# Kernel optimization log

Measured on AMD Instinct MI355X. Metric: run time of the kernel, lower is better.

## Reference

```python
import jax, jax.numpy as jnp
import numpy as np

HID = 256   # hidden_size
NH = 8      # n_heads
DH = HID // NH  # head dim = 32
NV = 20     # num_variables
B, T = 32, 512
EPS = 1e-5


def _ln(x, g, b):
    mu = jnp.mean(x, axis=-1, keepdims=True)
    var = jnp.mean(jnp.square(x - mu), axis=-1, keepdims=True)
    return (x - mu) * jax.lax.rsqrt(var + EPS) * g + b


def setup_inputs() -> dict:
    key = jax.random.key(0)
    ks = jax.random.split(key, 20)
    s = 0.05  # xavier-ish scale for random weights
    return {
        "x": jax.random.normal(ks[0], (B, T, NV, HID), dtype=jnp.float32),
        "cls_token": jax.random.normal(ks[1], (HID,), dtype=jnp.float32) * s,
        "wq": jax.random.normal(ks[2], (HID, HID), dtype=jnp.float32) * s,
        "bq": jnp.zeros((HID,), jnp.float32),
        "wk": jax.random.normal(ks[3], (HID, HID), dtype=jnp.float32) * s,
        "bk": jnp.zeros((HID,), jnp.float32),
        "wv": jax.random.normal(ks[4], (HID, HID), dtype=jnp.float32) * s,
        "bv": jnp.zeros((HID,), jnp.float32),
        "wo": jax.random.normal(ks[5], (HID, HID), dtype=jnp.float32) * s,
        "bo": jnp.zeros((HID,), jnp.float32),
        "ln1_g": jnp.ones((HID,), jnp.float32),
        "ln1_b": jnp.zeros((HID,), jnp.float32),
        "w1": jax.random.normal(ks[6], (HID, 4 * HID), dtype=jnp.float32) * s,
        "b1": jnp.zeros((4 * HID,), jnp.float32),
        "w2": jax.random.normal(ks[7], (4 * HID, HID), dtype=jnp.float32) * s,
        "b2": jnp.zeros((HID,), jnp.float32),
        "ln2_g": jnp.ones((HID,), jnp.float32),
        "ln2_b": jnp.zeros((HID,), jnp.float32),
        "ww": jax.random.normal(ks[8], (HID, NV), dtype=jnp.float32) * s,
        "bw": jnp.zeros((NV,), jnp.float32),
    }


def reference(x, cls_token, wq, bq, wk, bk, wv, bv, wo, bo,
              ln1_g, ln1_b, w1, b1, w2, b2, ln2_g, ln2_b, ww, bw):
    # x: [B, T, V, H] -- stacked pre-projected variables (input_size == hidden_size,
    # so the torch module has no per-variable projections).
    b, t = x.shape[0], x.shape[1]
    scale = 1.0 / np.sqrt(DH)

    # Cross-attention: query = cls token (len 1), keys/values = variables (len V).
    # No static_context, so the query is shared across (b, t).
    q = (cls_token @ wq + bq).reshape(NH, DH)            # [H] -> [nh, dh]
    k = (x @ wk + bk).reshape(b, t, NV, NH, DH)          # [B,T,V,nh,dh]
    v = (x @ wv + bv).reshape(b, t, NV, NH, DH)
    scores = jnp.einsum('hd,btvhd->bthv', q, k) * scale  # [B,T,nh,V]
    attn = jax.nn.softmax(scores, axis=-1)
    ctx = jnp.einsum('bthv,btvhd->bthd', attn, v).reshape(b, t, HID)
    attn_out = ctx @ wo + bo                             # [B,T,H]

    # FF block: LN -> Linear(4H) -> GELU -> Linear(H) -> LN (dropout is eval no-op)
    h = _ln(attn_out, ln1_g, ln1_b)
    h = jax.nn.gelu(h @ w1 + b1, approximate=False)
    h = h @ w2 + b2
    processed = _ln(h, ln2_g, ln2_b)                     # [B,T,H]

    weights = jax.nn.softmax(processed @ ww + bw, axis=-1)   # [B,T,V]
    vs_output = jnp.einsum('btv,btvh->bth', weights, x)      # [B,T,H]
    return vs_output, weights
```

## Files before the change

### kernel.cpp

```cpp
#include <hip/hip_runtime.h>
#include <hip/hip_bf16.h>
#include <math.h>

#define BT   16384
#define HIDS 256
#define NHS  8
#define NVS  20

typedef __attribute__((ext_vector_type(8))) short short8;
typedef __attribute__((ext_vector_type(4))) float floatx4;

__device__ __forceinline__ float bf2f(unsigned int u) {
    union { unsigned int u; float f; } cv; cv.u = u << 16; return cv.f;
}
__device__ __forceinline__ unsigned short f2bf(float f) {
    union { __hip_bfloat16 h; unsigned short u; } cv; cv.h = __float2bfloat16(f); return cv.u;
}
__device__ __forceinline__ unsigned int pk2(float a, float b) {
    return (unsigned int)f2bf(a) | ((unsigned int)f2bf(b) << 16);
}
__device__ __forceinline__ void gload16(const void* g, void* l) {
    __builtin_amdgcn_global_load_lds(
        (const __attribute__((address_space(1))) unsigned int*)g,
        (__attribute__((address_space(3))) unsigned int*)l, 16, 0, 0);
}

__global__ __launch_bounds__(256) void k_fold(
        const float* __restrict__ cls, const float* __restrict__ wq,
        const float* __restrict__ bq, const float* __restrict__ wk,
        const float* __restrict__ bk, unsigned short* __restrict__ qkbT,
        float* __restrict__ qb) {
    __shared__ float s_q[HIDS];
    int tid = threadIdx.x;
    float acc = bq[tid];
    for (int c = 0; c < HIDS; ++c) acc += cls[c] * wq[c * HIDS + tid];
    s_q[tid] = acc;
    __syncthreads();
    int c = tid;
    #pragma unroll
    for (int h = 0; h < NHS; ++h) {
        float a = 0.f;
        #pragma unroll
        for (int d = 0; d < 32; ++d) a += wk[c * HIDS + h * 32 + d] * s_q[h * 32 + d];
        qkbT[h * HIDS + c] = f2bf(a);
    }
    #pragma unroll
    for (int h = NHS; h < 16; ++h) qkbT[h * HIDS + c] = 0;
    if (tid < NHS) {
        float a = 0.f;
        #pragma unroll
        for (int d = 0; d < 32; ++d) a += bk[tid * 32 + d] * s_q[tid * 32 + d];
        qb[tid] = a;
    }
}

__global__ __launch_bounds__(256) void k_bvo(
        const float* __restrict__ bv, const float* __restrict__ wo,
        const float* __restrict__ bo, float* __restrict__ bvo) {
    int j = threadIdx.x;
    float a = bo[j];
    for (int i = 0; i < HIDS; ++i) a += bv[i] * wo[i * HIDS + j];
    bvo[j] = a;
}

__global__ __launch_bounds__(256) void k_wvo(
        const float* __restrict__ wv, const float* __restrict__ wo,
        unsigned short* __restrict__ wvo_t) {
    int hc = blockIdx.x; int h = hc >> 8, c = hc & 255;
    __shared__ float s_wv[32];
    int tid = threadIdx.x;
    if (tid < 32) s_wv[tid] = wv[c * HIDS + h * 32 + tid];
    __syncthreads();
    float a = 0.f;
    #pragma unroll 8
    for (int d = 0; d < 32; ++d) a += s_wv[d] * wo[(h * 32 + d) * HIDS + tid];
    wvo_t[(size_t)tid * 2048 + hc] = f2bf(a);
}

__global__ __launch_bounds__(256) void k_transp(const float* __restrict__ in,
        unsigned short* __restrict__ out, int R, int C) {
    __shared__ float s[32][36];
    int tid = threadIdx.x;
    int ct = blockIdx.x * 32, rt = blockIdx.y * 32;
    int r = tid >> 3, c4 = (tid & 7) * 4;
    float4 f = *(const float4*)&in[(size_t)(rt + r) * C + ct + c4];
    s[r][c4] = f.x; s[r][c4 + 1] = f.y; s[r][c4 + 2] = f.z; s[r][c4 + 3] = f.w;
    __syncthreads();
    int ro = tid >> 3, k4 = (tid & 7) * 4;
    ushort4 o;
    o.x = f2bf(s[k4][ro]);     o.y = f2bf(s[k4 + 1][ro]);
    o.z = f2bf(s[k4 + 2][ro]); o.w = f2bf(s[k4 + 3][ro]);
    *(ushort4*)&out[(size_t)(ct + ro) * R + rt + k4] = o;
}

__global__ __launch_bounds__(256) void k_attn(
        const float* __restrict__ x, const unsigned short* __restrict__ qkbT,
        const float* __restrict__ qb, unsigned short* __restrict__ xmix) {
    __shared__ __align__(16) unsigned short sX[92 * 256];
    __shared__ float s_at[4][NVS][NHS];
    int tid = threadIdx.x;
    int wave = tid >> 6, lane = tid & 63;
    int m = lane & 15, g = lane >> 4;
    size_t t0 = (size_t)blockIdx.x * 4;

    short8 qf[8];
    #pragma unroll
    for (int kk = 0; kk < 8; ++kk)
        qf[kk] = *(const short8*)&qkbT[m * HIDS + kk * 32 + g * 8];

    const float* xg = x + t0 * (NVS * HIDS);
    #pragma unroll
    for (int i = 0; i < 10; ++i) {
        int s = i * 256 + tid;
        int row = s >> 5, cc = s & 31;
        float4 f0 = *(const float4*)(xg + s * 8);
        float4 f1 = *(const float4*)(xg + s * 8 + 4);
        uint4 pk;
        pk.x = pk2(f0.x, f0.y); pk.y = pk2(f0.z, f0.w);
        pk.z = pk2(f1.x, f1.y); pk.w = pk2(f1.z, f1.w);
        int c = cc ^ (row & 7);
        *(uint4*)&sX[row * 256 + c * 8] = pk;
    }
    __syncthreads();

    int rbase = wave * NVS;
    floatx4 sc0 = {0.f, 0.f, 0.f, 0.f}, sc1 = {0.f, 0.f, 0.f, 0.f};
    #pragma unroll
    for (int kk = 0; kk < 8; ++kk) {
        int r0 = rbase + m;
        int c0 = (kk * 4 + g) ^ (r0 & 7);
        short8 a0 = *(const short8*)&sX[r0 * 256 + c0 * 8];
        int r1 = rbase + 16 + m;
        int c1 = (kk * 4 + g) ^ (r1 & 7);
        short8 a1 = *(const short8*)&sX[r1 * 256 + c1 * 8];
        sc0 = __builtin_amdgcn_mfma_f32_16x16x32_bf16(a0, qf[kk], sc0, 0, 0, 0);
        sc1 = __builtin_amdgcn_mfma_f32_16x16x32_bf16(a1, qf[kk], sc1, 0, 0, 0);
    }
    if (m < NHS) {
        #pragma unroll
        for (int r = 0; r < 4; ++r) s_at[wave][g * 4 + r][m] = sc0[r];
        if (g == 0) {
            #pragma unroll
            for (int r = 0; r < 4; ++r) s_at[wave][16 + r][m] = sc1[r];
        }
    }
    __syncthreads();

    if (lane < NHS) {
        float qbh = qb[lane];
        float sv[NVS]; float mx = -1e30f;
        #pragma unroll
        for (int v = 0; v < NVS; ++v) {
            float sc = (s_at[wave][v][lane] + qbh) * 0.17677669529663687f;
            sv[v] = sc; mx = fmaxf(mx, sc);
        }
        float sum = 0.f;
        #pragma unroll
        for (int v = 0; v < NVS; ++v) { sv[v] = expf(sv[v] - mx); sum += sv[v]; }
        float inv = 1.f / sum;
        #pragma unroll
        for (int v = 0; v < NVS; ++v) s_at[wave][v][lane] = sv[v] * inv;
    }
    __syncthreads();

    floatx4 acc[NHS];
    #pragma unroll
    for (int h = 0; h < NHS; ++h) acc[h] = (floatx4){0.f, 0.f, 0.f, 0.f};
    #pragma unroll
    for (int v = 0; v < NVS; ++v) {
        int r = rbase + v;
        int cidx = (((lane >> 1) ^ (r & 7)) << 3) + ((lane & 1) << 2);
        uint2 u = *(const uint2*)&sX[r * 256 + cidx];
        float x0 = bf2f(u.x & 0xffffu), x1 = bf2f(u.x >> 16);
        float x2 = bf2f(u.y & 0xffffu), x3 = bf2f(u.y >> 16);
        float4 w0 = *(const float4*)&s_at[wave][v][0];
        float4 w1 = *(const float4*)&s_at[wave][v][4];
        float wv8[8] = {w0.x, w0.y, w0.z, w0.w, w1.x, w1.y, w1.z, w1.w};
        #pragma unroll
        for (int h = 0; h < NHS; ++h) {
            acc[h][0] += wv8[h] * x0; acc[h][1] += wv8[h] * x1;
            acc[h][2] += wv8[h] * x2; acc[h][3] += wv8[h] * x3;
        }
    }
    unsigned short* op = xmix + (t0 + wave) * 2048;
    #pragma unroll
    for (int h = 0; h < NHS; ++h) {
        uint2 o; o.x = pk2(acc[h][0], acc[h][1]); o.y = pk2(acc[h][2], acc[h][3]);
        *(uint2*)&op[h * 256 + lane * 4] = o;
    }
}

template <int K, int N, int BN, bool GELU, bool OUT_BF16>
__global__ __launch_bounds__(256) void k_mgemm(
        const unsigned short* __restrict__ A,
        const unsigned short* __restrict__ Bt,
        const float* __restrict__ bias, void* __restrict__ outp) {
    constexpr int BM = 128, BK = 64;
    constexpr int NJ = BN / 32;
    __shared__ __align__(16) unsigned short sA[BM * BK];
    __shared__ __align__(16) unsigned short sB[BN * BK];
    int tid = threadIdx.x;
    int wave = tid >> 6, lane = tid & 63;
    int m = lane & 15, g = lane >> 4;
    int wm = (wave & 1) * 64, wn = (wave >> 1) * (BN / 2);
    size_t t0 = (size_t)blockIdx.x * BM;
    int n0 = blockIdx.y * BN;

    floatx4 acc[4][NJ];
    #pragma unroll
    for (int i = 0; i < 4; ++i)
        #pragma unroll
        for (int j = 0; j < NJ; ++j) acc[i][j] = (floatx4){0.f, 0.f, 0.f, 0.f};

    for (int k0 = 0; k0 < K; k0 += BK) {
        __syncthreads();
        #pragma unroll
        for (int i = 0; i < 4; ++i) {
            int s = i * 256 + tid;
            int row = s >> 3, cc = s & 7;
            int gc = cc ^ (row & 7);
            gload16(A + (t0 + row) * K + k0 + gc * 8, (char*)sA + s * 16);
        }
        #pragma unroll
        for (int i = 0; i < BN / 32; ++i) {
            int s = i * 256 + tid;
            int row = s >> 3, cc = s & 7;
            int gc = cc ^ (row & 7);
            gload16(Bt + (size_t)(n0 + row) * K + k0 + gc * 8, (char*)sB + s * 16);
        }
        __syncthreads();
        #pragma unroll
        for (int kk = 0; kk < 2; ++kk) {
            short8 af[4]; short8 bfr[NJ];
            #pragma unroll
            for (int i = 0; i < 4; ++i) {
                int row = wm + i * 16 + m;
                int c = (kk * 4 + g) ^ (row & 7);
                af[i] = *(const short8*)&sA[row * BK + c * 8];
            }
            #pragma unroll
            for (int j = 0; j < NJ; ++j) {
                int row = wn + j * 16 + m;
                int c = (kk * 4 + g) ^ (row & 7);
                bfr[j] = *(const short8*)&sB[row * BK + c * 8];
            }
            #pragma unroll
            for (int i = 0; i < 4; ++i)
                #pragma unroll
                for (int j = 0; j < NJ; ++j)
                    acc[i][j] = __builtin_amdgcn_mfma_f32_16x16x32_bf16(af[i], bfr[j], acc[i][j], 0, 0, 0);
        }
    }
    float bj[NJ];
    #pragma unroll
    for (int j = 0; j < NJ; ++j) bj[j] = bias[n0 + wn + j * 16 + m];
    #pragma unroll
    for (int i = 0; i < 4; ++i) {
        #pragma unroll
        for (int r = 0; r < 4; ++r) {
            size_t grow = t0 + wm + i * 16 + g * 4 + r;
            #pragma unroll
            for (int j = 0; j < NJ; ++j) {
                float v = acc[i][j][r] + bj[j];
                if (GELU) v = 0.5f * v * (1.f + erff(v * 0.70710678118654752f));
                if (OUT_BF16) {
                    float v2 = __shfl_xor(v, 1);
                    if (!(lane & 1)) {
                        *(unsigned int*)((unsigned short*)outp + grow * N + n0 + wn + j * 16 + m) = pk2(v, v2);
                    }
                } else {
                    ((float*)outp)[grow * N + n0 + wn + j * 16 + m] = v;
                }
            }
        }
    }
}

template <bool OUT_BF16>
__global__ __launch_bounds__(256) void k_ln(
        const float* __restrict__ in, const float* __restrict__ g,
        const float* __restrict__ b, void* __restrict__ outp) {
    int tid = threadIdx.x;
    size_t t = (size_t)blockIdx.x * 4 + (tid >> 6);
    int l = tid & 63;
    float4 v = ((const float4*)(in + t * HIDS))[l];
    float s = v.x + v.y + v.z + v.w;
    float sq = v.x * v.x + v.y * v.y + v.z * v.z + v.w * v.w;
    #pragma unroll
    for (int mm = 1; mm < 64; mm <<= 1) {
        s += __shfl_xor(s, mm, 64);
        sq += __shfl_xor(sq, mm, 64);
    }
    float mean = s * (1.f / HIDS);
    float var = sq * (1.f / HIDS) - mean * mean;
    float rstd = rsqrtf(var + 1e-5f);
    float4 g4 = ((const float4*)g)[l];
    float4 b4 = ((const float4*)b)[l];
    float ox = (v.x - mean) * rstd * g4.x + b4.x;
    float oy = (v.y - mean) * rstd * g4.y + b4.y;
    float oz = (v.z - mean) * rstd * g4.z + b4.z;
    float ow = (v.w - mean) * rstd * g4.w + b4.w;
    if (OUT_BF16) {
        uint2 o; o.x = pk2(ox, oy); o.y = pk2(oz, ow);
        *(uint2*)((unsigned short*)outp + t * HIDS + l * 4) = o;
    } else {
        float4 o; o.x = ox; o.y = oy; o.z = oz; o.w = ow;
        ((float4*)((float*)outp + t * HIDS))[l] = o;
    }
}

__global__ __launch_bounds__(256) void k_wsoft(
        const float* __restrict__ in, const float* __restrict__ lng,
        const float* __restrict__ lnb, const float* __restrict__ ww,
        const float* __restrict__ bw, float* __restrict__ wout) {
    __shared__ float s_p[16][HIDS + 1];
    __shared__ float s_red[2][16][16];
    __shared__ float s_ms[16][2];
    __shared__ float s_lg[16][NVS];
    int tid = threadIdx.x;
    size_t t0 = (size_t)blockIdx.x * 16;
    #pragma unroll
    for (int i = 0; i < 4; ++i) {
        int idx4 = i * 256 + tid;
        float4 f = ((const float4*)(in + t0 * HIDS))[idx4];
        int flat = idx4 * 4;
        int r = flat >> 8, c = flat & 255;
        s_p[r][c] = f.x; s_p[r][c + 1] = f.y; s_p[r][c + 2] = f.z; s_p[r][c + 3] = f.w;
    }
    __syncthreads();
    int r = tid >> 4, jg = tid & 15;
    float sum = 0.f, sq = 0.f;
    #pragma unroll
    for (int i = 0; i < 16; ++i) {
        float a = s_p[r][jg * 16 + i]; sum += a; sq += a * a;
    }
    s_red[0][r][jg] = sum; s_red[1][r][jg] = sq;
    __syncthreads();
    if (jg == 0) {
        float ts = 0.f, tq = 0.f;
        #pragma unroll
        for (int i = 0; i < 16; ++i) { ts += s_red[0][r][i]; tq += s_red[1][r][i]; }
        float mean = ts * (1.f / HIDS);
        float var = tq * (1.f / HIDS) - mean * mean;
        s_ms[r][0] = mean; s_ms[r][1] = rsqrtf(var + 1e-5f);
    }
    __syncthreads();
    float mean = s_ms[r][0], rstd = s_ms[r][1];
    #pragma unroll
    for (int i = 0; i < 16; ++i) {
        int c = jg * 16 + i;
        s_p[r][c] = (s_p[r][c] - mean) * rstd * lng[c] + lnb[c];
    }
    __syncthreads();
    if (jg < 10) {
        int o = jg * 2;
        float a0 = bw[o], a1 = bw[o + 1];
        #pragma unroll 4
        for (int c = 0; c < HIDS; ++c) {
            float a = s_p[r][c];
            const float2 w = *(const float2*)(ww + c * NVS + o);
            a0 += a * w.x; a1 += a * w.y;
        }
        s_lg[r][o] = a0; s_lg[r][o + 1] = a1;
    }
    __syncthreads();
    if (tid < 16) {
        int rr = tid;
        float mx = -1e30f;
        #pragma unroll
        for (int v = 0; v < NVS; ++v) mx = fmaxf(mx, s_lg[rr][v]);
        float e[NVS]; float ssum = 0.f;
        #pragma unroll
        for (int v = 0; v < NVS; ++v) { e[v] = expf(s_lg[rr][v] - mx); ssum += e[v]; }
        float inv = 1.f / ssum;
        #pragma unroll
        for (int v = 0; v < NVS; ++v) wout[(t0 + rr) * NVS + v] = e[v] * inv;
    }
}

__global__ __launch_bounds__(256) void k_vsout(
        const float* __restrict__ x, const float* __restrict__ wts,
        float* __restrict__ outp) {
    int tid = threadIdx.x;
    size_t t = (size_t)blockIdx.x * 4 + (tid >> 6);
    int l = tid & 63;
    const float4* xt = (const float4*)(x + t * (NVS * HIDS));
    const float* wr = wts + t * NVS;
    float4 acc = make_float4(0.f, 0.f, 0.f, 0.f);
    #pragma unroll
    for (int v = 0; v < NVS; ++v) {
        float w = wr[v];
        float4 a = xt[v * 64 + l];
        acc.x += w * a.x; acc.y += w * a.y; acc.z += w * a.z; acc.w += w * a.w;
    }
    ((float4*)(outp + t * HIDS))[l] = acc;
}

extern "C" void kernel_launch(void* const* d_in, const int* in_sizes, int n_in,
                              void* d_out, int out_size, void* d_ws, size_t ws_size,
                              hipStream_t stream) {
    const float* x     = (const float*)d_in[0];
    const float* cls   = (const float*)d_in[1];
    const float* wq    = (const float*)d_in[2];
    const float* bq    = (const float*)d_in[3];
    const float* wk    = (const float*)d_in[4];
    const float* bk    = (const float*)d_in[5];
    const float* wv    = (const float*)d_in[6];
    const float* bv    = (const float*)d_in[7];
    const float* wo    = (const float*)d_in[8];
    const float* bo    = (const float*)d_in[9];
    const float* ln1_g = (const float*)d_in[10];
    const float* ln1_b = (const float*)d_in[11];
    const float* w1    = (const float*)d_in[12];
    const float* b1    = (const float*)d_in[13];
    const float* w2    = (const float*)d_in[14];
    const float* b2    = (const float*)d_in[15];
    const float* ln2_g = (const float*)d_in[16];
    const float* ln2_b = (const float*)d_in[17];
    const float* ww    = (const float*)d_in[18];
    const float* bw    = (const float*)d_in[19];

    float* outf   = (float*)d_out;
    float* vs_out = outf;
    float* w_out  = outf + (size_t)BT * HIDS;

    char* ws = (char*)d_ws;
    unsigned short* qkbT = (unsigned short*)ws;
    float* qb   = (float*)(ws + 8192);
    float* bvo  = (float*)(ws + 8448);
    unsigned short* w1t   = (unsigned short*)(ws + 16384);
    unsigned short* w2t   = (unsigned short*)(ws + 16384 + 524288);
    unsigned short* wvo_t = (unsigned short*)(ws + 16384 + 1048576);
    char* big = ws + 16384 + 1048576 + 1048576;
    unsigned short* bufA = (unsigned short*)big;
    float* buf1 = (float*)(big + (size_t)BT * 2048 * 2);
    unsigned short* hb = (unsigned short*)(big + (size_t)BT * 2048 * 2 + (size_t)BT * HIDS * 4);

    k_fold<<<1, 256, 0, stream>>>(cls, wq, bq, wk, bk, qkbT, qb);
    k_bvo<<<1, 256, 0, stream>>>(bv, wo, bo, bvo);
    k_wvo<<<2048, 256, 0, stream>>>(wv, wo, wvo_t);
    k_transp<<<dim3(32, 8), 256, 0, stream>>>(w1, w1t, 256, 1024);
    k_transp<<<dim3(8, 32), 256, 0, stream>>>(w2, w2t, 1024, 256);

    k_attn<<<BT / 4, 256, 0, stream>>>(x, qkbT, qb, bufA);
    k_mgemm<2048, 256, 64, false, false><<<dim3(128, 4), 256, 0, stream>>>(bufA, wvo_t, bvo, buf1);
    k_ln<true><<<BT / 4, 256, 0, stream>>>(buf1, ln1_g, ln1_b, hb);
    k_mgemm<256, 1024, 128, true, true><<<dim3(128, 8), 256, 0, stream>>>(hb, w1t, b1, bufA);
    k_mgemm<1024, 256, 64, false, false><<<dim3(128, 4), 256, 0, stream>>>(bufA, w2t, b2, buf1);
    k_wsoft<<<BT / 16, 256, 0, stream>>>(buf1, ln2_g, ln2_b, ww, bw, w_out);
    k_vsout<<<BT / 4, 256, 0, stream>>>(x, w_out, vs_out);
}
```

Measured before the change: 742.2 us.

## Fuse LayerNorm into GEMM epilogue, merge weight-softmax with output mixing, restructure GEMM tiles

Replaces the 128xBN GEMM with a 32x256 tile so each block owns full 256-wide rows. That lets the first LayerNorm run inside the GEMM epilogue, which removes the separate k_ln pass and an fp32 round trip. The weight softmax and the weighted sum over x now share one kernel, so the separate vs-out launch and the reread of the weights are gone. k_wvo is also rewritten to use far fewer blocks with reuse through shared memory. The risk is that the smaller M tile lowers MFMA reuse, and the B tile is reloaded by four times as many blocks.

```diff
diff --git a/kernel.cpp b/kernel.cpp
--- a/kernel.cpp
+++ b/kernel.cpp
@@ -66,15 +66,31 @@
 __global__ __launch_bounds__(256) void k_wvo(
         const float* __restrict__ wv, const float* __restrict__ wo,
         unsigned short* __restrict__ wvo_t) {
-    int hc = blockIdx.x; int h = hc >> 8, c = hc & 255;
-    __shared__ float s_wv[32];
+    int h = blockIdx.x >> 2;
+    int j0 = (blockIdx.x & 3) * 64;
     int tid = threadIdx.x;
-    if (tid < 32) s_wv[tid] = wv[c * HIDS + h * 32 + tid];
-    __syncthreads();
-    float a = 0.f;
-    #pragma unroll 8
-    for (int d = 0; d < 32; ++d) a += s_wv[d] * wo[(h * 32 + d) * HIDS + tid];
-    wvo_t[(size_t)tid * 2048 + hc] = f2bf(a);
+    __shared__ float s_wo[32][64];
+    #pragma unroll
+    for (int i = 0; i < 8; ++i) {
+        int idx = i * 256 + tid;
+        int d = idx >> 6, jj = idx & 63;
+        s_wo[d][jj] = wo[(h * 32 + d) * HIDS + j0 + jj];
+    }
+    float av[32];
+    #pragma unroll
+    for (int d4 = 0; d4 < 8; ++d4) {
+        float4 f = *(const float4*)(wv + (size_t)tid * HIDS + h * 32 + d4 * 4);
+        av[d4 * 4] = f.x; av[d4 * 4 + 1] = f.y;
+        av[d4 * 4 + 2] = f.z; av[d4 * 4 + 3] = f.w;
+    }
+    __syncthreads();
+    #pragma unroll 4
+    for (int jj = 0; jj < 64; ++jj) {
+        float a = 0.f;
+        #pragma unroll
+        for (int d = 0; d < 32; ++d) a += av[d] * s_wo[d][jj];
+        wvo_t[(size_t)(j0 + jj) * 2048 + h * 256 + tid] = f2bf(a);
+    }
 }
 
 __global__ __launch_bounds__(256) void k_transp(const float* __restrict__ in,
@@ -190,39 +206,40 @@
     }
 }
 
-template <int K, int N, int BN, bool GELU, bool OUT_BF16>
-__global__ __launch_bounds__(256) void k_mgemm(
+template <int K, int NTOT, bool GELU, bool LN, bool OUTF32>
+__global__ __launch_bounds__(256) void k_mg(
         const unsigned short* __restrict__ A,
         const unsigned short* __restrict__ Bt,
-        const float* __restrict__ bias, void* __restrict__ outp) {
-    constexpr int BM = 128, BK = 64;
-    constexpr int NJ = BN / 32;
+        const float* __restrict__ bias,
+        const float* __restrict__ lng, const float* __restrict__ lnb,
+        void* __restrict__ outp) {
+    constexpr int BM = 32, BK = 64;
     __shared__ __align__(16) unsigned short sA[BM * BK];
-    __shared__ __align__(16) unsigned short sB[BN * BK];
+    __shared__ __align__(16) unsigned short sB[256 * BK];
+    __shared__ float s_sum[4][BM], s_sq[4][BM], s_ms[BM][2];
     int tid = threadIdx.x;
     int wave = tid >> 6, lane = tid & 63;
     int m = lane & 15, g = lane >> 4;
-    int wm = (wave & 1) * 64, wn = (wave >> 1) * (BN / 2);
+    int wn = wave * 64;
     size_t t0 = (size_t)blockIdx.x * BM;
-    int n0 = blockIdx.y * BN;
-
-    floatx4 acc[4][NJ];
-    #pragma unroll
-    for (int i = 0; i < 4; ++i)
-        #pragma unroll
-        for (int j = 0; j < NJ; ++j) acc[i][j] = (floatx4){0.f, 0.f, 0.f, 0.f};
+    int n0 = blockIdx.y * 256;
+
+    floatx4 acc[2][4];
+    #pragma unroll
+    for (int i = 0; i < 2; ++i)
+        #pragma unroll
+        for (int j = 0; j < 4; ++j) acc[i][j] = (floatx4){0.f, 0.f, 0.f, 0.f};
 
     for (int k0 = 0; k0 < K; k0 += BK) {
         __syncthreads();
-        #pragma unroll
-        for (int i = 0; i < 4; ++i) {
-            int s = i * 256 + tid;
+        {
+            int s = tid;
             int row = s >> 3, cc = s & 7;
             int gc = cc ^ (row & 7);
             gload16(A + (t0 + row) * K + k0 + gc * 8, (char*)sA + s * 16);
         }
         #pragma unroll
-        for (int i = 0; i < BN / 32; ++i) {
+        for (int i = 0; i < 8; ++i) {
             int s = i * 256 + tid;
             int row = s >> 3, cc = s & 7;
             int gc = cc ^ (row & 7);
@@ -231,92 +248,124 @@
         __syncthreads();
         #pragma unroll
         for (int kk = 0; kk < 2; ++kk) {
-            short8 af[4]; short8 bfr[NJ];
-            #pragma unroll
-            for (int i = 0; i < 4; ++i) {
-                int row = wm + i * 16 + m;
+            short8 af[2]; short8 bfr[4];
+            #pragma unroll
+            for (int i = 0; i < 2; ++i) {
+                int row = i * 16 + m;
                 int c = (kk * 4 + g) ^ (row & 7);
                 af[i] = *(const short8*)&sA[row * BK + c * 8];
             }
             #pragma unroll
-            for (int j = 0; j < NJ; ++j) {
+            for (int j = 0; j < 4; ++j) {
                 int row = wn + j * 16 + m;
                 int c = (kk * 4 + g) ^ (row & 7);
                 bfr[j] = *(const short8*)&sB[row * BK + c * 8];
             }
             #pragma unroll
-            for (int i = 0; i < 4; ++i)
+            for (int i = 0; i < 2; ++i)
                 #pragma unroll
-                for (int j = 0; j < NJ; ++j)
+                for (int j = 0; j < 4; ++j)
                     acc[i][j] = __builtin_amdgcn_mfma_f32_16x16x32_bf16(af[i], bfr[j], acc[i][j], 0, 0, 0);
         }
     }
-    float bj[NJ];
-    #pragma unroll
-    for (int j = 0; j < NJ; ++j) bj[j] = bias[n0 + wn + j * 16 + m];
-    #pragma unroll
-    for (int i = 0; i < 4; ++i) {
+
+    float vv[2][4][4];
+    #pragma unroll
+    for (int j = 0; j < 4; ++j) {
+        float bj = bias[n0 + wn + j * 16 + m];
+        #pragma unroll
+        for (int i = 0; i < 2; ++i)
+            #pragma unroll
+            for (int r = 0; r < 4; ++r) {
+                float v = acc[i][j][r] + bj;
+                if (GELU) v = 0.5f * v * (1.f + erff(v * 0.70710678118654752f));
+                vv[i][j][r] = v;
+            }
+    }
+
+    if (LN) {
+        float ps[2][4], pq[2][4];
+        #pragma unroll
+        for (int i = 0; i < 2; ++i)
+            #pragma unroll
+            for (int r = 0; r < 4; ++r) {
+                float s = 0.f, q = 0.f;
+                #pragma unroll
+                for (int j = 0; j < 4; ++j) { float v = vv[i][j][r]; s += v; q += v * v; }
+                #pragma unroll
+                for (int mk = 1; mk < 16; mk <<= 1) {
+                    s += __shfl_xor(s, mk, 64);
+                    q += __shfl_xor(q, mk, 64);
+                }
+                ps[i][r] = s; pq[i][r] = q;
+            }
+        if ((lane & 15) == 0) {
+            #pragma unroll
+            for (int i = 0; i < 2; ++i)
+                #pragma unroll
+                for (int r = 0; r < 4; ++r) {
+                    int row = i * 16 + g * 4 + r;
+                    s_sum[wave][row] = ps[i][r];
+                    s_sq[wave][row] = pq[i][r];
+                }
+        }
+        __syncthreads();
+        if (tid < BM) {
+            float ts = 0.f, tq = 0.f;
+            #pragma unroll
+            for (int w = 0; w < 4; ++w) { ts += s_sum[w][tid]; tq += s_sq[w][tid]; }
+            float mean = ts * (1.f / 256.f);
+            float var = tq * (1.f / 256.f) - mean * mean;
+            s_ms[tid][0] = mean; s_ms[tid][1] = rsqrtf(var + 1e-5f);
+        }
+        __syncthreads();
+        float lg[4], lb[4];
+        #pragma unroll
+        for (int j = 0; j < 4; ++j) {
+            lg[j] = lng[wn + j * 16 + m];
+            lb[j] = lnb[wn + j * 16 + m];
+        }
+        #pragma unroll
+        for (int i = 0; i < 2; ++i)
+            #pragma unroll
+            for (int r = 0; r < 4; ++r) {
+                int row = i * 16 + g * 4 + r;
+                float mean = s_ms[row][0], rstd = s_ms[row][1];
+                #pragma unroll
+                for (int j = 0; j < 4; ++j)
+                    vv[i][j][r] = (vv[i][j][r] - mean) * rstd * lg[j] + lb[j];
+            }
+    }
+
+    #pragma unroll
+    for (int i = 0; i < 2; ++i)
         #pragma unroll
         for (int r = 0; r < 4; ++r) {
-            size_t grow = t0 + wm + i * 16 + g * 4 + r;
-            #pragma unroll
-            for (int j = 0; j < NJ; ++j) {
-                float v = acc[i][j][r] + bj[j];
-                if (GELU) v = 0.5f * v * (1.f + erff(v * 0.70710678118654752f));
-                if (OUT_BF16) {
+            size_t grow = t0 + i * 16 + g * 4 + r;
+            #pragma unroll
+            for (int j = 0; j < 4; ++j) {
+                float v = vv[i][j][r];
+                if (OUTF32) {
+                    ((float*)outp)[grow * NTOT + n0 + wn + j * 16 + m] = v;
+                } else {
                     float v2 = __shfl_xor(v, 1);
-                    if (!(lane & 1)) {
-                        *(unsigned int*)((unsigned short*)outp + grow * N + n0 + wn + j * 16 + m) = pk2(v, v2);
-                    }
-                } else {
-                    ((float*)outp)[grow * N + n0 + wn + j * 16 + m] = v;
+                    if (!(lane & 1))
+                        *(unsigned int*)((unsigned short*)outp + grow * NTOT + n0 + wn + j * 16 + m) = pk2(v, v2);
                 }
             }
         }
-    }
-}
-
-template <bool OUT_BF16>
-__global__ __launch_bounds__(256) void k_ln(
-        const float* __restrict__ in, const float* __restrict__ g,
-        const float* __restrict__ b, void* __restrict__ outp) {
-    int tid = threadIdx.x;
-    size_t t = (size_t)blockIdx.x * 4 + (tid >> 6);
-    int l = tid & 63;
-    float4 v = ((const float4*)(in + t * HIDS))[l];
-    float s = v.x + v.y + v.z + v.w;
-    float sq = v.x * v.x + v.y * v.y + v.z * v.z + v.w * v.w;
-    #pragma unroll
-    for (int mm = 1; mm < 64; mm <<= 1) {
-        s += __shfl_xor(s, mm, 64);
-        sq += __shfl_xor(sq, mm, 64);
-    }
-    float mean = s * (1.f / HIDS);
-    float var = sq * (1.f / HIDS) - mean * mean;
-    float rstd = rsqrtf(var + 1e-5f);
-    float4 g4 = ((const float4*)g)[l];
-    float4 b4 = ((const float4*)b)[l];
-    float ox = (v.x - mean) * rstd * g4.x + b4.x;
-    float oy = (v.y - mean) * rstd * g4.y + b4.y;
-    float oz = (v.z - mean) * rstd * g4.z + b4.z;
-    float ow = (v.w - mean) * rstd * g4.w + b4.w;
-    if (OUT_BF16) {
-        uint2 o; o.x = pk2(ox, oy); o.y = pk2(oz, ow);
-        *(uint2*)((unsigned short*)outp + t * HIDS + l * 4) = o;
-    } else {
-        float4 o; o.x = ox; o.y = oy; o.z = oz; o.w = ow;
-        ((float4*)((float*)outp + t * HIDS))[l] = o;
-    }
-}
-
-__global__ __launch_bounds__(256) void k_wsoft(
+}
+
+__global__ __launch_bounds__(256) void k_wsel(
         const float* __restrict__ in, const float* __restrict__ lng,
         const float* __restrict__ lnb, const float* __restrict__ ww,
-        const float* __restrict__ bw, float* __restrict__ wout) {
+        const float* __restrict__ bw, const float* __restrict__ x,
+        float* __restrict__ wout, float* __restrict__ vs_out) {
     __shared__ float s_p[16][HIDS + 1];
     __shared__ float s_red[2][16][16];
     __shared__ float s_ms[16][2];
     __shared__ float s_lg[16][NVS];
+    __shared__ float s_w[16][NVS];
     int tid = threadIdx.x;
     size_t t0 = (size_t)blockIdx.x * 16;
     #pragma unroll
@@ -374,26 +423,27 @@
         for (int v = 0; v < NVS; ++v) { e[v] = expf(s_lg[rr][v] - mx); ssum += e[v]; }
         float inv = 1.f / ssum;
         #pragma unroll
-        for (int v = 0; v < NVS; ++v) wout[(t0 + rr) * NVS + v] = e[v] * inv;
-    }
-}
-
-__global__ __launch_bounds__(256) void k_vsout(
-        const float* __restrict__ x, const float* __restrict__ wts,
-        float* __restrict__ outp) {
-    int tid = threadIdx.x;
-    size_t t = (size_t)blockIdx.x * 4 + (tid >> 6);
-    int l = tid & 63;
-    const float4* xt = (const float4*)(x + t * (NVS * HIDS));
-    const float* wr = wts + t * NVS;
-    float4 acc = make_float4(0.f, 0.f, 0.f, 0.f);
-    #pragma unroll
-    for (int v = 0; v < NVS; ++v) {
-        float w = wr[v];
-        float4 a = xt[v * 64 + l];
-        acc.x += w * a.x; acc.y += w * a.y; acc.z += w * a.z; acc.w += w * a.w;
-    }
-    ((float4*)(outp + t * HIDS))[l] = acc;
+        for (int v = 0; v < NVS; ++v) {
+            float wv_ = e[v] * inv;
+            s_w[rr][v] = wv_;
+            wout[(t0 + rr) * NVS + v] = wv_;
+        }
+    }
+    __syncthreads();
+    int wave = tid >> 6, l = tid & 63;
+    #pragma unroll
+    for (int tt = 0; tt < 4; ++tt) {
+        int t = wave * 4 + tt;
+        const float4* xt = (const float4*)(x + (t0 + t) * (NVS * HIDS));
+        float4 acc = make_float4(0.f, 0.f, 0.f, 0.f);
+        #pragma unroll
+        for (int v = 0; v < NVS; ++v) {
+            float w = s_w[t][v];
+            float4 a = xt[v * 64 + l];
+            acc.x += w * a.x; acc.y += w * a.y; acc.z += w * a.z; acc.w += w * a.w;
+        }
+        ((float4*)(vs_out + (t0 + t) * HIDS))[l] = acc;
+    }
 }
 
 extern "C" void kernel_launch(void* const* d_in, const int* in_sizes, int n_in,
@@ -433,20 +483,21 @@
     unsigned short* wvo_t = (unsigned short*)(ws + 16384 + 1048576);
     char* big = ws + 16384 + 1048576 + 1048576;
     unsigned short* bufA = (unsigned short*)big;
-    float* buf1 = (float*)(big + (size_t)BT * 2048 * 2);
-    unsigned short* hb = (unsigned short*)(big + (size_t)BT * 2048 * 2 + (size_t)BT * HIDS * 4);
+    unsigned short* hb   = (unsigned short*)(big + (size_t)BT * 2048 * 2);
+    float* buf1 = (float*)(big + (size_t)BT * 2048 * 2 + (size_t)BT * HIDS * 2);
 
     k_fold<<<1, 256, 0, stream>>>(cls, wq, bq, wk, bk, qkbT, qb);
     k_bvo<<<1, 256, 0, stream>>>(bv, wo, bo, bvo);
-    k_wvo<<<2048, 256, 0, stream>>>(wv, wo, wvo_t);
+    k_wvo<<<32, 256, 0, stream>>>(wv, wo, wvo_t);
     k_transp<<<dim3(32, 8), 256, 0, stream>>>(w1, w1t, 256, 1024);
     k_transp<<<dim3(8, 32), 256, 0, stream>>>(w2, w2t, 1024, 256);
 
     k_attn<<<BT / 4, 256, 0, stream>>>(x, qkbT, qb, bufA);
-    k_mgemm<2048, 256, 64, false, false><<<dim3(128, 4), 256, 0, stream>>>(bufA, wvo_t, bvo, buf1);
-    k_ln<true><<<BT / 4, 256, 0, stream>>>(buf1, ln1_g, ln1_b, hb);
-    k_mgemm<256, 1024, 128, true, true><<<dim3(128, 8), 256, 0, stream>>>(hb, w1t, b1, bufA);
-    k_mgemm<1024, 256, 64, false, false><<<dim3(128, 4), 256, 0, stream>>>(bufA, w2t, b2, buf1);
-    k_wsoft<<<BT / 16, 256, 0, stream>>>(buf1, ln2_g, ln2_b, ww, bw, w_out);
-    k_vsout<<<BT / 4, 256, 0, stream>>>(x, w_out, vs_out);
-}
+    k_mg<2048, 256, false, true, false><<<dim3(BT / 32, 1), 256, 0, stream>>>(
+        bufA, wvo_t, bvo, ln1_g, ln1_b, hb);
+    k_mg<256, 1024, true, false, false><<<dim3(BT / 32, 4), 256, 0, stream>>>(
+        hb, w1t, b1, nullptr, nullptr, bufA);
+    k_mg<1024, 256, false, false, true><<<dim3(BT / 32, 1), 256, 0, stream>>>(
+        bufA, w2t, b2, nullptr, nullptr, buf1);
+    k_wsel<<<BT / 16, 256, 0, stream>>>(buf1, ln2_g, ln2_b, ww, bw, x, w_out, vs_out);
+}
```

After: 742.8 us. Within noise of the previous version (+0.1%).
